# Kernel optimization log

Measured on AMD Instinct MI355X. Metric: run time of the kernel, lower is better.

## Reference

```python
import jax, jax.numpy as jnp
import numpy as np

DIM = 2048
HV = 32          # num value heads
HK = 16          # num key heads
DK = 128         # head_k_dim
DV = 128         # head_v_dim
KW = 4           # conv kernel width
KEY_DIM = HK * DK            # 2048
VAL_DIM = HV * DV            # 4096
CONV_DIM = 2 * KEY_DIM + VAL_DIM  # 8192
EPS = 1e-6
B, T = 2, 2048


def setup_inputs() -> dict:
    key = jax.random.key(0)
    ks = jax.random.split(key, 10)
    s = 0.02
    x = jax.random.normal(ks[0], (B, T, DIM), jnp.float32)
    W_qkv = jax.random.normal(ks[1], (DIM, CONV_DIM), jnp.float32) * s
    W_z = jax.random.normal(ks[2], (DIM, VAL_DIM), jnp.float32) * s
    W_a = jax.random.normal(ks[3], (DIM, HV), jnp.float32) * s
    W_b = jax.random.normal(ks[4], (DIM, HV), jnp.float32) * s
    W_out = jax.random.normal(ks[5], (VAL_DIM, DIM), jnp.float32) * s
    conv_w = jax.random.normal(ks[6], (CONV_DIM, KW), jnp.float32) * 0.2
    A_log = jnp.log(jax.random.uniform(ks[7], (HV,), jnp.float32, 1e-3, 16.0))
    dt_bias = jnp.ones((HV,), jnp.float32)
    norm_weight = jnp.ones((DV,), jnp.float32)
    return {"x": x, "W_qkv": W_qkv, "W_z": W_z, "W_a": W_a, "W_b": W_b,
            "W_out": W_out, "conv_w": conv_w, "dt_bias": dt_bias,
            "A_log": A_log, "norm_weight": norm_weight}


def _l2norm(t):
    return t * jax.lax.rsqrt(jnp.sum(t * t, axis=-1, keepdims=True) + EPS)


def _forward(x, W_qkv, W_z, W_a, W_b, W_out, conv_w, dt_bias, A_log, norm_weight):
    Bb, Tt, _ = x.shape
    mixed = x @ W_qkv                       # [B,T,CONV_DIM]
    z = x @ W_z                             # [B,T,VAL_DIM]
    a = x @ W_a                             # [B,T,HV]
    b = x @ W_b                             # [B,T,HV]

    # depthwise causal conv1d (left pad KW-1) + silu
    xp = jnp.pad(mixed, ((0, 0), (KW - 1, 0), (0, 0)))
    conv = sum(xp[:, i:i + Tt, :] * conv_w[:, i] for i in range(KW))
    mixed = jax.nn.silu(conv)

    q, k, v = jnp.split(mixed, [KEY_DIM, 2 * KEY_DIM], axis=-1)
    q = q.reshape(Bb, Tt, HK, DK)
    k = k.reshape(Bb, Tt, HK, DK)
    v = v.reshape(Bb, Tt, HV, DV)
    rep = HV // HK
    q = jnp.repeat(q, rep, axis=2)          # [B,T,HV,DK]
    k = jnp.repeat(k, rep, axis=2)

    # decay / beta
    beta = jax.nn.sigmoid(b)                                    # [B,T,HV]
    g = -jnp.exp(A_log) * jax.nn.softplus(a + dt_bias)          # [B,T,HV], < 0

    # qk l2norm in kernel + scale
    q = _l2norm(q) * (DK ** -0.5)
    k = _l2norm(k)

    # gated delta rule recurrence, time-major scan
    qT = q.transpose(1, 0, 2, 3)
    kT = k.transpose(1, 0, 2, 3)
    vT = v.transpose(1, 0, 2, 3)
    gT = g.transpose(1, 0, 2)
    bT = beta.transpose(1, 0, 2)
    S0 = jnp.zeros((Bb, HV, DK, DV), jnp.float32)

    def step(S, inp):
        qt, kt, vt, gt, bt = inp
        S = S * jnp.exp(gt)[..., None, None]
        pred = jnp.einsum('bhk,bhkv->bhv', kt, S)
        u = (vt - pred) * bt[..., None]
        S = S + jnp.einsum('bhk,bhv->bhkv', kt, u)
        o = jnp.einsum('bhk,bhkv->bhv', qt, S)
        return S, o

    _, oT = jax.lax.scan(step, S0, (qT, kT, vT, gT, bT))
    o = oT.transpose(1, 0, 2, 3)            # [B,T,HV,DV]

    # gated RMSNorm over head_v_dim: weight * rmsnorm(o) * silu(z)
    var = jnp.mean(o * o, axis=-1, keepdims=True)
    on = o * jax.lax.rsqrt(var + EPS) * norm_weight
    zg = z.reshape(Bb, Tt, HV, DV)
    on = on * jax.nn.silu(zg)

    return on.reshape(Bb, Tt, VAL_DIM) @ W_out


def reference(x, W_qkv, W_z, W_a, W_b, W_out, conv_w, dt_bias, A_log, norm_weight):
    return _forward(x, W_qkv, W_z, W_a, W_b, W_out, conv_w, dt_bias, A_log, norm_weight)
```

## Files before the change

kernel.cpp:

```cpp
#include <hip/hip_runtime.h>
#include <hip/hip_bf16.h>
#include <cstdint>
#include <cstddef>

#define DIM_ 2048
#define HV_ 32
#define HK_ 16
#define DK_ 128
#define DV_ 128
#define KW_ 4
#define KEY_DIM_ 2048
#define VAL_DIM_ 4096
#define CONV_DIM_ 8192
#define B_ 2
#define T_ 2048
#define BT_ 4096
#define CH_ 64
#define NC_ (T_ / CH_)

typedef short s8v __attribute__((ext_vector_type(8)));
typedef float f4v __attribute__((ext_vector_type(4)));

__device__ __forceinline__ unsigned short f2b(float f) {
    union { float f; unsigned u; } c; c.f = f;
    unsigned u = c.u;
    return (unsigned short)((u + 0x7fffu + ((u >> 16) & 1u)) >> 16);
}
__device__ __forceinline__ float b2f(unsigned short s) {
    union { unsigned u; float f; } c; c.u = ((unsigned)s) << 16;
    return c.f;
}
__device__ __forceinline__ unsigned int pk2(float a, float b) {
    return (unsigned)f2b(a) | ((unsigned)f2b(b) << 16);
}
__device__ __forceinline__ float silu(float x) { return x / (1.f + expf(-x)); }

__global__ void cast_bf16_k(const float* __restrict__ in, unsigned short* __restrict__ out, int n8) {
    int i = blockIdx.x * blockDim.x + threadIdx.x;
    if (i >= n8) return;
    int base = i * 8;
    f4v a = *(const f4v*)(in + base);
    f4v b = *(const f4v*)(in + base + 4);
    s8v o;
    o[0] = (short)f2b(a[0]); o[1] = (short)f2b(a[1]); o[2] = (short)f2b(a[2]); o[3] = (short)f2b(a[3]);
    o[4] = (short)f2b(b[0]); o[5] = (short)f2b(b[1]); o[6] = (short)f2b(b[2]); o[7] = (short)f2b(b[3]);
    *(s8v*)(out + base) = o;
}

__global__ void transpose_cast_k(const float* __restrict__ in, unsigned short* __restrict__ out,
                                 int R, int C) {
    __shared__ float tile[32][33];
    int c0 = blockIdx.x * 32, r0 = blockIdx.y * 32;
    int tx = threadIdx.x & 31, ty = threadIdx.x >> 5;
#pragma unroll
    for (int j = 0; j < 32; j += 8)
        tile[ty + j][tx] = in[(size_t)(r0 + ty + j) * C + c0 + tx];
    __syncthreads();
#pragma unroll
    for (int j = 0; j < 32; j += 8)
        out[(size_t)(c0 + ty + j) * R + r0 + tx] = f2b(tile[tx][ty + j]);
}

template <int OUT_BF16>
__global__ __launch_bounds__(256) void gemm_bt_k(const unsigned short* __restrict__ A,
                                                 const unsigned short* __restrict__ BT,
                                                 void* __restrict__ Cv,
                                                 int M, int N, int K) {
    __shared__ __attribute__((aligned(16))) unsigned short As[128 * 64];
    __shared__ __attribute__((aligned(16))) unsigned short Bs[128 * 64];
    const int tid = threadIdx.x;
    const int wid = tid >> 6, lane = tid & 63;
    const int wm = wid >> 1, wn = wid & 1;
    const int m0 = blockIdx.y * 128, n0 = blockIdx.x * 128;

    f4v acc[4][4];
#pragma unroll
    for (int i = 0; i < 4; i++)
#pragma unroll
        for (int j = 0; j < 4; j++) acc[i][j] = (f4v){0.f, 0.f, 0.f, 0.f};

    const int rowA = tid >> 3;
    const int cb   = (tid & 7) << 4;

    for (int kt = 0; kt < K; kt += 64) {
#pragma unroll
        for (int i = 0; i < 4; i++) {
            int row = i * 32 + rowA;
            int scb = cb ^ ((row & 7) << 4);
            const unsigned short* ga = A  + (size_t)(m0 + row) * K + kt + (scb >> 1);
            const unsigned short* gb = BT + (size_t)(n0 + row) * K + kt + (scb >> 1);
            char* la = (char*)As + i * 4096 + (wid << 10);
            char* lb = (char*)Bs + i * 4096 + (wid << 10);
            __builtin_amdgcn_global_load_lds(
                (const __attribute__((address_space(1))) unsigned int*)ga,
                (__attribute__((address_space(3))) unsigned int*)la, 16, 0, 0);
            __builtin_amdgcn_global_load_lds(
                (const __attribute__((address_space(1))) unsigned int*)gb,
                (__attribute__((address_space(3))) unsigned int*)lb, 16, 0, 0);
        }
        __syncthreads();
#pragma unroll
        for (int kk = 0; kk < 2; kk++) {
            s8v af[4], bfr[4];
#pragma unroll
            for (int mi = 0; mi < 4; mi++) {
                int row = wm * 64 + mi * 16 + (lane & 15);
                int byteoff = (row << 7) + ((kk * 64 + ((lane >> 4) << 4)) ^ ((row & 7) << 4));
                af[mi] = *(const s8v*)((const char*)As + byteoff);
            }
#pragma unroll
            for (int ni = 0; ni < 4; ni++) {
                int row = wn * 64 + ni * 16 + (lane & 15);
                int byteoff = (row << 7) + ((kk * 64 + ((lane >> 4) << 4)) ^ ((row & 7) << 4));
                bfr[ni] = *(const s8v*)((const char*)Bs + byteoff);
            }
#pragma unroll
            for (int mi = 0; mi < 4; mi++)
#pragma unroll
                for (int ni = 0; ni < 4; ni++)
                    acc[mi][ni] = __builtin_amdgcn_mfma_f32_16x16x32_bf16(
                        af[mi], bfr[ni], acc[mi][ni], 0, 0, 0);
        }
        __syncthreads();
    }
#pragma unroll
    for (int mi = 0; mi < 4; mi++) {
#pragma unroll
        for (int ni = 0; ni < 4; ni++) {
            int row = m0 + wm * 64 + mi * 16 + ((lane >> 4) << 2);
            int col = n0 + wn * 64 + ni * 16 + (lane & 15);
#pragma unroll
            for (int r = 0; r < 4; r++) {
                float v = acc[mi][ni][r];
                if (OUT_BF16)
                    ((unsigned short*)Cv)[(size_t)(row + r) * N + col] = f2b(v);
                else
                    ((float*)Cv)[(size_t)(row + r) * N + col] = v;
            }
        }
    }
}

__global__ __launch_bounds__(256) void ab_gbeta_k(const float* __restrict__ x,
                                                  const float* __restrict__ Wa,
                                                  const float* __restrict__ Wb,
                                                  const float* __restrict__ dt_bias,
                                                  const float* __restrict__ A_log,
                                                  float* __restrict__ g, float* __restrict__ beta) {
    __shared__ float xr0[16 * 513];
    const int tid = threadIdx.x;
    const int r = tid & 15, cc = tid >> 4;
    const int row0 = blockIdx.x * 16;
    float a0 = 0.f, a1 = 0.f, b0 = 0.f, b1 = 0.f;
    for (int kc = 0; kc < 2048; kc += 512) {
#pragma unroll
        for (int q = 0; q < 8; q++) {
            int f = q * 256 + tid;
            int rw = f >> 7, cl = (f & 127) << 2;
            *(f4v*)&xr0[rw * 513 + cl] = *(const f4v*)(x + (size_t)(row0 + rw) * 2048 + kc + cl);
        }
        __syncthreads();
#pragma unroll 8
        for (int k = 0; k < 512; k++) {
            float xv = xr0[r * 513 + k];
            size_t kk = (size_t)(kc + k) * 32;
            a0 += xv * Wa[kk + cc];
            a1 += xv * Wa[kk + cc + 16];
            b0 += xv * Wb[kk + cc];
            b1 += xv * Wb[kk + cc + 16];
        }
        __syncthreads();
    }
    int row = row0 + r;
    float av0 = a0 + dt_bias[cc], av1 = a1 + dt_bias[cc + 16];
    float sp0 = (av0 > 20.f) ? av0 : log1pf(expf(av0));
    float sp1 = (av1 > 20.f) ? av1 : log1pf(expf(av1));
    g[(size_t)row * 32 + cc]      = -expf(A_log[cc]) * sp0;
    g[(size_t)row * 32 + cc + 16] = -expf(A_log[cc + 16]) * sp1;
    beta[(size_t)row * 32 + cc]      = 1.f / (1.f + expf(-b0));
    beta[(size_t)row * 32 + cc + 16] = 1.f / (1.f + expf(-b1));
}

__global__ __launch_bounds__(256) void conv_fused_k(const unsigned short* __restrict__ mixp,
                                                    const float* __restrict__ convw,
                                                    unsigned short* __restrict__ qn,
                                                    unsigned short* __restrict__ kn,
                                                    unsigned short* __restrict__ vv) {
    int btid = blockIdx.x;
    int t = btid & (T_ - 1);
    int c = (blockIdx.y << 9) + (threadIdx.x << 1);
    const unsigned short* base = mixp + (size_t)btid * CONV_DIM_ + c;
    unsigned m3 = *(const unsigned*)(base);
    unsigned m2 = (t >= 1) ? *(const unsigned*)(base - CONV_DIM_) : 0u;
    unsigned m1 = (t >= 2) ? *(const unsigned*)(base - 2 * CONV_DIM_) : 0u;
    unsigned m0 = (t >= 3) ? *(const unsigned*)(base - 3 * CONV_DIM_) : 0u;
    f4v w0 = *(const f4v*)(convw + (size_t)c * 4);
    f4v w1 = *(const f4v*)(convw + (size_t)c * 4 + 4);
    float v0 = b2f((unsigned short)(m3 & 0xffff)) * w0[3] + b2f((unsigned short)(m2 & 0xffff)) * w0[2]
             + b2f((unsigned short)(m1 & 0xffff)) * w0[1] + b2f((unsigned short)(m0 & 0xffff)) * w0[0];
    float v1 = b2f((unsigned short)(m3 >> 16)) * w1[3] + b2f((unsigned short)(m2 >> 16)) * w1[2]
             + b2f((unsigned short)(m1 >> 16)) * w1[1] + b2f((unsigned short)(m0 >> 16)) * w1[0];
    v0 = silu(v0); v1 = silu(v1);
    if (c < 2 * KEY_DIM_) {
        float ss = v0 * v0 + v1 * v1;
#pragma unroll
        for (int m = 1; m < 64; m <<= 1) ss += __shfl_xor(ss, m);
        float scale = rsqrtf(ss + 1e-6f);
        int head = (c >> 7) & 15, d = c & 127;
        if (c < KEY_DIM_) {
            scale *= 0.08838834764831845f;
            *(unsigned*)(qn + ((size_t)btid * HK_ + head) * DK_ + d) = pk2(v0 * scale, v1 * scale);
        } else {
            *(unsigned*)(kn + ((size_t)btid * HK_ + head) * DK_ + d) = pk2(v0 * scale, v1 * scale);
        }
    } else {
        *(unsigned*)(vv + (size_t)btid * VAL_DIM_ + (c - 2 * KEY_DIM_)) = pk2(v0, v1);
    }
}

__global__ __launch_bounds__(256) void chunk_pre_k(
    const unsigned short* __restrict__ qn, const unsigned short* __restrict__ kn,
    unsigned short* __restrict__ vv,
    const float* __restrict__ g, const float* __restrict__ beta,
    unsigned short* __restrict__ Wg, unsigned short* __restrict__ Aog,
    unsigned short* __restrict__ knT, float* __restrict__ expG, float* __restrict__ expGr)
{
    const int c = blockIdx.x, h = blockIdx.y, b = blockIdx.z;
    const int hk = h >> 1;
    const int tid = threadIdx.x, wid = tid >> 6, lane = tid & 63;
    const int r15 = lane & 15, g4 = lane >> 4;

    __shared__ __attribute__((aligned(16))) unsigned short Klds[64 * 128];
    __shared__ __attribute__((aligned(16))) unsigned short Xlds[128 * 64];
    __shared__ float AT[64][68];
    __shared__ float STmp[16][17];
    __shared__ float Gl[64], Bl[64], EG[64];

    const size_t t0 = (size_t)b * T_ + (size_t)c * 64;
    const size_t cbk = ((size_t)(b * 32 + h) * 32 + c);

#pragma unroll
    for (int p = 0; p < 4; p++) {
        int row = p * 16 + (tid >> 4);
        int colB = (tid & 15) << 4;
        int sw = colB ^ ((row & 7) << 4);
        s8v kv = *(const s8v*)(kn + ((t0 + row) * HK_ + hk) * DK_ + (colB >> 1));
        *(s8v*)((char*)Klds + row * 256 + sw) = kv;
        s8v qv = *(const s8v*)(qn + ((t0 + row) * HK_ + hk) * DK_ + (colB >> 1));
        *(s8v*)((char*)Xlds + row * 256 + sw) = qv;
    }
    if (tid < 64) {
        Gl[tid] = g[(t0 + tid) * HV_ + h];
        Bl[tid] = beta[(t0 + tid) * HV_ + h];
    }
    __syncthreads();
    if (tid == 0) {
        float s = 0.f;
        for (int i = 0; i < 64; i++) { s += Gl[i]; Gl[i] = s; }
    }
    __syncthreads();
    if (tid < 64) {
        float Gi = Gl[tid], Gn = Gl[63];
        float e1 = expf(Gi), e2 = expf(Gn - Gi);
        EG[tid] = e1;
        expG[cbk * 64 + tid] = e1;
        expGr[cbk * 64 + tid] = e2;
    }
    __syncthreads();

    f4v kkv[4], qkv[4];
#pragma unroll
    for (int jt = 0; jt < 4; jt++) { kkv[jt] = (f4v){0,0,0,0}; qkv[jt] = (f4v){0,0,0,0}; }
    const int arow = wid * 16 + r15;
#pragma unroll
    for (int ks = 0; ks < 4; ks++) {
        int abyte = arow * 256 + ((ks * 64 + (g4 << 4)) ^ ((arow & 7) << 4));
        s8v ak = *(const s8v*)((const char*)Klds + abyte);
        s8v aq = *(const s8v*)((const char*)Xlds + abyte);
#pragma unroll
        for (int jt = 0; jt < 4; jt++) {
            int jrow = jt * 16 + r15;
            int bbyte = jrow * 256 + ((ks * 64 + (g4 << 4)) ^ ((jrow & 7) << 4));
            s8v bk = *(const s8v*)((const char*)Klds + bbyte);
            kkv[jt] = __builtin_amdgcn_mfma_f32_16x16x32_bf16(ak, bk, kkv[jt], 0, 0, 0);
            qkv[jt] = __builtin_amdgcn_mfma_f32_16x16x32_bf16(aq, bk, qkv[jt], 0, 0, 0);
        }
    }
#pragma unroll
    for (int jt = 0; jt < 4; jt++) {
#pragma unroll
        for (int r = 0; r < 4; r++) {
            int i = wid * 16 + g4 * 4 + r;
            int j = jt * 16 + r15;
            float em = expf(fminf(Gl[i] - Gl[j], 0.f));
            AT[i][j] = (j < i) ? Bl[i] * em * kkv[jt][r] : 0.f;
            float ao = (j <= i) ? em * qkv[jt][r] : 0.f;
            Aog[cbk * 4096 + i * 64 + j] = f2b(ao);
        }
    }
    __syncthreads();

    for (int u = tid; u < 1024; u += 256) {
        int row = u >> 4, v0i = (u & 15) << 3;
        s8v vx = *(const s8v*)(vv + (t0 + row) * VAL_DIM_ + h * 128 + v0i);
        float bt = Bl[row];
#pragma unroll
        for (int e = 0; e < 8; e++) {
            int v = v0i + e;
            *(unsigned short*)((char*)Xlds + v * 128 + ((row * 2) ^ ((v & 7) << 4))) =
                f2b(b2f((unsigned short)vx[e]) * bt);
        }
    }
    if ((h & 1) == 0) {
        int dk = tid & 127, th = (tid >> 7) << 5;
        size_t basek = ((size_t)(b * 16 + hk) * 128 + dk) * (size_t)T_ + (size_t)c * 64 + th;
#pragma unroll
        for (int t8 = 0; t8 < 4; t8++) {
            s8v kv;
#pragma unroll
            for (int e = 0; e < 8; e++) {
                int tt = th + t8 * 8 + e;
                kv[e] = (short)*(const unsigned short*)((const char*)Klds + tt * 256 + ((dk * 2) ^ ((tt & 7) << 4)));
            }
            *(s8v*)(knT + basek + t8 * 8) = kv;
        }
    }
    __syncthreads();

    if (lane < 16) {
        int r0 = wid * 16, col = lane;
#pragma unroll
        for (int i = 0; i < 16; i++) {
            float s = 0.f;
            for (int j = 0; j < i; j++) s += AT[r0 + i][r0 + j] * AT[r0 + j][r0 + col];
            AT[r0 + i][r0 + col] = ((col == i) ? 1.f : 0.f) - s;
        }
    }
    __syncthreads();

    {
        int ii = tid >> 4, jj = tid & 15;
        for (int I = 1; I < 4; I++)
            for (int J = 0; J < I; J++) {
                float s = 0.f;
                for (int K = J; K < I; K++) {
#pragma unroll
                    for (int m = 0; m < 16; m++)
                        s += AT[16 * I + ii][16 * K + m] * AT[16 * K + m][16 * J + jj];
                }
                STmp[ii][jj] = s;
                __syncthreads();
                float y = 0.f;
#pragma unroll
                for (int m = 0; m < 16; m++) y += AT[16 * I + ii][16 * I + m] * STmp[m][jj];
                __syncthreads();
                AT[16 * I + ii][16 * J + jj] = -y;
                __syncthreads();
            }
    }

    f4v tb[8];
#pragma unroll
    for (int vt = 0; vt < 8; vt++) tb[vt] = (f4v){0,0,0,0};
#pragma unroll
    for (int ks = 0; ks < 2; ks++) {
        s8v ta;
#pragma unroll
        for (int e = 0; e < 8; e++) ta[e] = (short)f2b(AT[arow][ks * 32 + g4 * 8 + e]);
#pragma unroll
        for (int vt = 0; vt < 8; vt++) {
            int v = vt * 16 + r15;
            int bbyte = v * 128 + ((ks * 64 + (g4 << 4)) ^ ((v & 7) << 4));
            s8v bv = *(const s8v*)((const char*)Xlds + bbyte);
            tb[vt] = __builtin_amdgcn_mfma_f32_16x16x32_bf16(ta, bv, tb[vt], 0, 0, 0);
        }
    }
#pragma unroll
    for (int vt = 0; vt < 8; vt++)
#pragma unroll
        for (int r = 0; r < 4; r++) {
            int i = wid * 16 + g4 * 4 + r, v = vt * 16 + r15;
            vv[(t0 + i) * VAL_DIM_ + h * 128 + v] = f2b(tb[vt][r]);
        }
    __syncthreads();

    {
        int dk = tid & 127;
        int tb0 = (tid >> 7) << 5;
#pragma unroll
        for (int t8 = 0; t8 < 4; t8++) {
            int tbase = tb0 + t8 * 8;
            s8v kw;
#pragma unroll
            for (int e = 0; e < 8; e++) {
                int t = tbase + e;
                float kv = b2f(*(const unsigned short*)((const char*)Klds + t * 256 + ((dk * 2) ^ ((t & 7) << 4))));
                kw[e] = (short)f2b(kv * Bl[t] * EG[t]);
            }
            *(s8v*)((char*)Xlds + dk * 128 + ((tbase * 2) ^ ((dk & 7) << 4))) = kw;
        }
    }
    __syncthreads();

    f4v wm[8];
#pragma unroll
    for (int dt = 0; dt < 8; dt++) wm[dt] = (f4v){0,0,0,0};
#pragma unroll
    for (int ks = 0; ks < 2; ks++) {
        s8v ta;
#pragma unroll
        for (int e = 0; e < 8; e++) ta[e] = (short)f2b(AT[arow][ks * 32 + g4 * 8 + e]);
#pragma unroll
        for (int dt = 0; dt < 8; dt++) {
            int dkr = dt * 16 + r15;
            int bbyte = dkr * 128 + ((ks * 64 + (g4 << 4)) ^ ((dkr & 7) << 4));
            s8v bw = *(const s8v*)((const char*)Xlds + bbyte);
            wm[dt] = __builtin_amdgcn_mfma_f32_16x16x32_bf16(ta, bw, wm[dt], 0, 0, 0);
        }
    }
#pragma unroll
    for (int dt = 0; dt < 8; dt++)
#pragma unroll
        for (int r = 0; r < 4; r++) {
            int i = wid * 16 + g4 * 4 + r, dk = dt * 16 + r15;
            Wg[cbk * 8192 + i * 128 + dk] = f2b(wm[dt][r]);
        }
}

__global__ __launch_bounds__(256) void chunk_scan_k(
    const unsigned short* __restrict__ qn, const unsigned short* __restrict__ knT,
    const unsigned short* __restrict__ tbv,
    const unsigned short* __restrict__ Wg, const unsigned short* __restrict__ Aog,
    const float* __restrict__ expG, const float* __restrict__ expGr,
    unsigned short* __restrict__ ob)
{
    const int bx = blockIdx.x;
    const int vq = bx & 3, h = (bx >> 2) & 31, b = bx >> 7;
    const int hk = h >> 1;
    const int tid = threadIdx.x, wid = tid >> 6, lane = tid & 63;
    const int r15 = lane & 15, g4 = lane >> 4;

    __shared__ __attribute__((aligned(16))) unsigned short Slds[32 * 128];
    __shared__ __attribute__((aligned(16))) unsigned short Ulds[32 * 64];
    __shared__ __attribute__((aligned(16))) unsigned short Uplds[32 * 64];

    f4v S[2][2];
#pragma unroll
    for (int i = 0; i < 2; i++)
#pragma unroll
        for (int j = 0; j < 2; j++) S[i][j] = (f4v){0,0,0,0};

    for (int c = 0; c < NC_; c++) {
        const size_t cbk = ((size_t)(b * 32 + h) * 32 + c);
        const size_t t0 = (size_t)b * T_ + (size_t)c * 64;

#pragma unroll
        for (int dkt = 0; dkt < 2; dkt++)
#pragma unroll
            for (int vt = 0; vt < 2; vt++) {
                int v = vt * 16 + r15;
                int dkb = ((wid * 2 + dkt) * 16 + g4 * 4) * 2;
                int sw = (v & 7) << 4;
                *(unsigned int*)((char*)Slds + v * 256 + ((dkb) ^ sw))     = pk2(S[dkt][vt][0], S[dkt][vt][1]);
                *(unsigned int*)((char*)Slds + v * 256 + ((dkb + 4) ^ sw)) = pk2(S[dkt][vt][2], S[dkt][vt][3]);
            }
        __syncthreads();

        f4v P[2]; P[0] = (f4v){0,0,0,0}; P[1] = (f4v){0,0,0,0};
        s8v sf[4][2];
        const unsigned short* wp = Wg + cbk * 8192 + (size_t)(wid * 16 + r15) * 128;
#pragma unroll
        for (int ks = 0; ks < 4; ks++) {
            s8v aw = *(const s8v*)(wp + ks * 32 + g4 * 8);
#pragma unroll
            for (int vt = 0; vt < 2; vt++) {
                int v = vt * 16 + r15;
                sf[ks][vt] = *(const s8v*)((const char*)Slds + v * 256 + ((ks * 64 + g4 * 16) ^ ((v & 7) << 4)));
                P[vt] = __builtin_amdgcn_mfma_f32_16x16x32_bf16(aw, sf[ks][vt], P[vt], 0, 0, 0);
            }
        }
        float egr[4];
#pragma unroll
        for (int r = 0; r < 4; r++) egr[r] = expGr[cbk * 64 + wid * 16 + g4 * 4 + r];
#pragma unroll
        for (int vt = 0; vt < 2; vt++) {
            float uu[4], up[4];
#pragma unroll
            for (int r = 0; r < 4; r++) {
                int t = wid * 16 + g4 * 4 + r;
                unsigned short tv = tbv[(t0 + t) * VAL_DIM_ + h * 128 + vq * 32 + vt * 16 + r15];
                uu[r] = b2f(tv) - P[vt][r];
                up[r] = uu[r] * egr[r];
            }
            int v = vt * 16 + r15;
            int tb2 = (wid * 16 + g4 * 4) * 2;
            int sw = (v & 7) << 4;
            *(unsigned int*)((char*)Ulds  + v * 128 + ((tb2) ^ sw))     = pk2(uu[0], uu[1]);
            *(unsigned int*)((char*)Ulds  + v * 128 + ((tb2 + 4) ^ sw)) = pk2(uu[2], uu[3]);
            *(unsigned int*)((char*)Uplds + v * 128 + ((tb2) ^ sw))     = pk2(up[0], up[1]);
            *(unsigned int*)((char*)Uplds + v * 128 + ((tb2 + 4) ^ sw)) = pk2(up[2], up[3]);
        }
        __syncthreads();

        f4v O[2]; O[0] = (f4v){0,0,0,0}; O[1] = (f4v){0,0,0,0};
        float egi = expG[cbk * 64 + wid * 16 + r15];
        const unsigned short* qp = qn + ((t0 + wid * 16 + r15) * HK_ + hk) * DK_;
#pragma unroll
        for (int ks = 0; ks < 4; ks++) {
            s8v q0 = *(const s8v*)(qp + ks * 32 + g4 * 8);
            s8v qg;
#pragma unroll
            for (int e = 0; e < 8; e++) qg[e] = (short)f2b(b2f((unsigned short)q0[e]) * egi);
#pragma unroll
            for (int vt = 0; vt < 2; vt++)
                O[vt] = __builtin_amdgcn_mfma_f32_16x16x32_bf16(qg, sf[ks][vt], O[vt], 0, 0, 0);
        }
        const unsigned short* ap = Aog + cbk * 4096 + (size_t)(wid * 16 + r15) * 64;
#pragma unroll
        for (int ks = 0; ks < 2; ks++) {
            s8v aa = *(const s8v*)(ap + ks * 32 + g4 * 8);
#pragma unroll
            for (int vt = 0; vt < 2; vt++) {
                int v = vt * 16 + r15;
                s8v bu = *(const s8v*)((const char*)Ulds + v * 128 + ((ks * 64 + g4 * 16) ^ ((v & 7) << 4)));
                O[vt] = __builtin_amdgcn_mfma_f32_16x16x32_bf16(aa, bu, O[vt], 0, 0, 0);
            }
        }
#pragma unroll
        for (int vt = 0; vt < 2; vt++)
#pragma unroll
            for (int r = 0; r < 4; r++) {
                int t = c * 64 + wid * 16 + g4 * 4 + r;
                ob[((size_t)b * T_ + t) * VAL_DIM_ + h * 128 + vq * 32 + vt * 16 + r15] = f2b(O[vt][r]);
            }

        float gam = expG[cbk * 64 + 63];
#pragma unroll
        for (int dkt = 0; dkt < 2; dkt++)
#pragma unroll
            for (int vt = 0; vt < 2; vt++) {
                S[dkt][vt][0] *= gam; S[dkt][vt][1] *= gam;
                S[dkt][vt][2] *= gam; S[dkt][vt][3] *= gam;
            }
        const unsigned short* kp = knT + ((size_t)(b * 16 + hk) * 128) * (size_t)T_;
#pragma unroll
        for (int ks = 0; ks < 2; ks++) {
            s8v bu[2];
#pragma unroll
            for (int vt = 0; vt < 2; vt++) {
                int v = vt * 16 + r15;
                bu[vt] = *(const s8v*)((const char*)Uplds + v * 128 + ((ks * 64 + g4 * 16) ^ ((v & 7) << 4)));
            }
#pragma unroll
            for (int dkt = 0; dkt < 2; dkt++) {
                s8v ak = *(const s8v*)(kp + (size_t)((wid * 2 + dkt) * 16 + r15) * T_ + (size_t)c * 64 + ks * 32 + g4 * 8);
#pragma unroll
                for (int vt = 0; vt < 2; vt++)
                    S[dkt][vt] = __builtin_amdgcn_mfma_f32_16x16x32_bf16(ak, bu[vt], S[dkt][vt], 0, 0, 0);
            }
        }
        __syncthreads();
    }
}

__global__ __launch_bounds__(256) void norm_gate_k(unsigned short* __restrict__ o,
                                                   const unsigned short* __restrict__ z,
                                                   const float* __restrict__ nw) {
    int lane = threadIdx.x & 63;
    size_t bh = (size_t)blockIdx.x * 4 + (threadIdx.x >> 6);
    unsigned ov = *(unsigned*)(o + bh * 128 + lane * 2);
    float v0 = b2f((unsigned short)(ov & 0xffff)), v1 = b2f((unsigned short)(ov >> 16));
    float ss = v0 * v0 + v1 * v1;
#pragma unroll
    for (int m = 1; m < 64; m <<= 1) ss += __shfl_xor(ss, m);
    float rr = rsqrtf(ss * (1.f / 128.f) + 1e-6f);
    unsigned zv = *(const unsigned*)(z + bh * 128 + lane * 2);
    float z0 = b2f((unsigned short)(zv & 0xffff)), z1 = b2f((unsigned short)(zv >> 16));
    float o0 = v0 * rr * nw[lane * 2]     * silu(z0);
    float o1 = v1 * rr * nw[lane * 2 + 1] * silu(z1);
    *(unsigned*)(o + bh * 128 + lane * 2) = pk2(o0, o1);
}

extern "C" void kernel_launch(void* const* d_in, const int* in_sizes, int n_in,
                              void* d_out, int out_size, void* d_ws, size_t ws_size,
                              hipStream_t stream) {
    const float* x      = (const float*)d_in[0];
    const float* W_qkv  = (const float*)d_in[1];
    const float* W_z    = (const float*)d_in[2];
    const float* W_a    = (const float*)d_in[3];
    const float* W_b    = (const float*)d_in[4];
    const float* W_out  = (const float*)d_in[5];
    const float* conv_w = (const float*)d_in[6];
    const float* dt_bias= (const float*)d_in[7];
    const float* A_log  = (const float*)d_in[8];
    const float* norm_w = (const float*)d_in[9];

    char* w = (char*)d_ws;
    const size_t MBc = (size_t)1 << 20;
    unsigned short* mixp  = (unsigned short*)(w);
    unsigned short* Wmat  = (unsigned short*)(w);
    unsigned short* knT   = (unsigned short*)(w + 32 * MBc);
    unsigned short* Aog   = (unsigned short*)(w + 48 * MBc);
    unsigned short* WqkvT = (unsigned short*)(w + 64 * MBc);
    unsigned short* obuf  = (unsigned short*)(w + 64 * MBc);
    unsigned short* kn    = (unsigned short*)(w + 80 * MBc);
    unsigned short* WzT   = (unsigned short*)(w + 96 * MBc);
    unsigned short* WoutT = (unsigned short*)(w + 96 * MBc);
    unsigned short* xb    = (unsigned short*)(w + 112 * MBc);
    unsigned short* qn    = (unsigned short*)(w + 112 * MBc);
    unsigned short* vv    = (unsigned short*)(w + 128 * MBc);
    unsigned short* zb    = (unsigned short*)(w + 160 * MBc);
    float* gbuf  = (float*)(w + 192 * MBc);
    float* bbuf  = (float*)(w + 192 * MBc + 512 * 1024);
    float* expG  = (float*)(w + 192 * MBc + 1024 * 1024);
    float* expGr = (float*)(w + 192 * MBc + 1536 * 1024);

    cast_bf16_k<<<(BT_ * DIM_ / 8 + 255) / 256, 256, 0, stream>>>(x, xb, BT_ * DIM_ / 8);
    transpose_cast_k<<<dim3(CONV_DIM_ / 32, DIM_ / 32), 256, 0, stream>>>(W_qkv, WqkvT, DIM_, CONV_DIM_);
    transpose_cast_k<<<dim3(VAL_DIM_ / 32, DIM_ / 32), 256, 0, stream>>>(W_z, WzT, DIM_, VAL_DIM_);
    gemm_bt_k<1><<<dim3(CONV_DIM_ / 128, BT_ / 128), 256, 0, stream>>>(xb, WqkvT, mixp, BT_, CONV_DIM_, DIM_);
    gemm_bt_k<1><<<dim3(VAL_DIM_ / 128, BT_ / 128), 256, 0, stream>>>(xb, WzT, zb, BT_, VAL_DIM_, DIM_);
    transpose_cast_k<<<dim3(DIM_ / 32, VAL_DIM_ / 32), 256, 0, stream>>>(W_out, WoutT, VAL_DIM_, DIM_);
    ab_gbeta_k<<<BT_ / 16, 256, 0, stream>>>(x, W_a, W_b, dt_bias, A_log, gbuf, bbuf);
    conv_fused_k<<<dim3(BT_, CONV_DIM_ / 512), 256, 0, stream>>>(mixp, conv_w, qn, kn, vv);
    chunk_pre_k<<<dim3(NC_, HV_, B_), 256, 0, stream>>>(qn, kn, vv, gbuf, bbuf,
                                                        Wmat, Aog, knT, expG, expGr);
    chunk_scan_k<<<B_ * HV_ * 4, 256, 0, stream>>>(qn, knT, vv, Wmat, Aog, expG, expGr, obuf);
    norm_gate_k<<<BT_ * HV_ / 4, 256, 0, stream>>>(obuf, zb, norm_w);
    gemm_bt_k<0><<<dim3(DIM_ / 128, BT_ / 128), 256, 0, stream>>>(obuf, WoutT, d_out, BT_, DIM_, VAL_DIM_);
}
```

Baseline: 754.2 us.

## Prefetch next chunk operands in scan, fuse x cast into ab_gbeta, split QKV GEMM

The chunk scan loop is restructured to load the next chunk's global operands (W, A, k, q, v, decay factors) into registers while the current chunk computes, using two alternating operand sets. One __syncthreads per chunk is removed by moving a barrier. The bf16 cast of x is folded into ab_gbeta_k so the separate cast kernel disappears, and the QKV GEMM is launched as two half-width launches. Double-buffered registers raise VGPR pressure and may reduce occupancy, and the barrier removal needs the LDS reuse ordering to stay correct.

```diff
diff --git a/kernel.cpp b/kernel.cpp
--- a/kernel.cpp
+++ b/kernel.cpp
@@ -35,18 +35,6 @@
 }
 __device__ __forceinline__ float silu(float x) { return x / (1.f + expf(-x)); }
 
-__global__ void cast_bf16_k(const float* __restrict__ in, unsigned short* __restrict__ out, int n8) {
-    int i = blockIdx.x * blockDim.x + threadIdx.x;
-    if (i >= n8) return;
-    int base = i * 8;
-    f4v a = *(const f4v*)(in + base);
-    f4v b = *(const f4v*)(in + base + 4);
-    s8v o;
-    o[0] = (short)f2b(a[0]); o[1] = (short)f2b(a[1]); o[2] = (short)f2b(a[2]); o[3] = (short)f2b(a[3]);
-    o[4] = (short)f2b(b[0]); o[5] = (short)f2b(b[1]); o[6] = (short)f2b(b[2]); o[7] = (short)f2b(b[3]);
-    *(s8v*)(out + base) = o;
-}
-
 __global__ void transpose_cast_k(const float* __restrict__ in, unsigned short* __restrict__ out,
                                  int R, int C) {
     __shared__ float tile[32][33];
@@ -146,7 +134,8 @@
                                                   const float* __restrict__ Wb,
                                                   const float* __restrict__ dt_bias,
                                                   const float* __restrict__ A_log,
-                                                  float* __restrict__ g, float* __restrict__ beta) {
+                                                  float* __restrict__ g, float* __restrict__ beta,
+                                                  unsigned short* __restrict__ xb) {
     __shared__ float xr0[16 * 513];
     const int tid = threadIdx.x;
     const int r = tid & 15, cc = tid >> 4;
@@ -157,7 +146,11 @@
         for (int q = 0; q < 8; q++) {
             int f = q * 256 + tid;
             int rw = f >> 7, cl = (f & 127) << 2;
-            *(f4v*)&xr0[rw * 513 + cl] = *(const f4v*)(x + (size_t)(row0 + rw) * 2048 + kc + cl);
+            f4v xv = *(const f4v*)(x + (size_t)(row0 + rw) * 2048 + kc + cl);
+            *(f4v*)&xr0[rw * 513 + cl] = xv;
+            unsigned long long p = (unsigned long long)pk2(xv[0], xv[1])
+                                 | ((unsigned long long)pk2(xv[2], xv[3]) << 32);
+            *(unsigned long long*)(xb + (size_t)(row0 + rw) * 2048 + kc + cl) = p;
         }
         __syncthreads();
 #pragma unroll 8
@@ -450,10 +443,46 @@
 #pragma unroll
         for (int j = 0; j < 2; j++) S[i][j] = (f4v){0,0,0,0};
 
-    for (int c = 0; c < NC_; c++) {
+    struct ScanOps {
+        s8v aw[4], aa[2], ak[4], q0[4];
+        float tv[8], egr4[4], egi, gam;
+    };
+    ScanOps opA, opB;
+
+    const unsigned short* kpbase = knT + ((size_t)(b * 16 + hk) * 128) * (size_t)T_;
+
+    auto scan_load = [&](ScanOps& o, int c) {
         const size_t cbk = ((size_t)(b * 32 + h) * 32 + c);
         const size_t t0 = (size_t)b * T_ + (size_t)c * 64;
-
+        const unsigned short* wp = Wg + cbk * 8192 + (size_t)(wid * 16 + r15) * 128;
+#pragma unroll
+        for (int ks = 0; ks < 4; ks++) o.aw[ks] = *(const s8v*)(wp + ks * 32 + g4 * 8);
+        const unsigned short* ap = Aog + cbk * 4096 + (size_t)(wid * 16 + r15) * 64;
+#pragma unroll
+        for (int ks = 0; ks < 2; ks++) o.aa[ks] = *(const s8v*)(ap + ks * 32 + g4 * 8);
+#pragma unroll
+        for (int ks = 0; ks < 2; ks++)
+#pragma unroll
+            for (int dkt = 0; dkt < 2; dkt++)
+                o.ak[ks * 2 + dkt] = *(const s8v*)(kpbase +
+                    (size_t)((wid * 2 + dkt) * 16 + r15) * T_ + (size_t)c * 64 + ks * 32 + g4 * 8);
+        const unsigned short* qp = qn + ((t0 + wid * 16 + r15) * HK_ + hk) * DK_;
+#pragma unroll
+        for (int ks = 0; ks < 4; ks++) o.q0[ks] = *(const s8v*)(qp + ks * 32 + g4 * 8);
+#pragma unroll
+        for (int vt = 0; vt < 2; vt++)
+#pragma unroll
+            for (int r = 0; r < 4; r++) {
+                int t = wid * 16 + g4 * 4 + r;
+                o.tv[vt * 4 + r] = b2f(tbv[(t0 + t) * VAL_DIM_ + h * 128 + vq * 32 + vt * 16 + r15]);
+            }
+#pragma unroll
+        for (int r = 0; r < 4; r++) o.egr4[r] = expGr[cbk * 64 + wid * 16 + g4 * 4 + r];
+        o.egi = expG[cbk * 64 + wid * 16 + r15];
+        o.gam = expG[cbk * 64 + 63];
+    };
+
+    auto body = [&](ScanOps& o, int c) {
 #pragma unroll
         for (int dkt = 0; dkt < 2; dkt++)
 #pragma unroll
@@ -468,29 +497,21 @@
 
         f4v P[2]; P[0] = (f4v){0,0,0,0}; P[1] = (f4v){0,0,0,0};
         s8v sf[4][2];
-        const unsigned short* wp = Wg + cbk * 8192 + (size_t)(wid * 16 + r15) * 128;
-#pragma unroll
-        for (int ks = 0; ks < 4; ks++) {
-            s8v aw = *(const s8v*)(wp + ks * 32 + g4 * 8);
+#pragma unroll
+        for (int ks = 0; ks < 4; ks++)
 #pragma unroll
             for (int vt = 0; vt < 2; vt++) {
                 int v = vt * 16 + r15;
                 sf[ks][vt] = *(const s8v*)((const char*)Slds + v * 256 + ((ks * 64 + g4 * 16) ^ ((v & 7) << 4)));
-                P[vt] = __builtin_amdgcn_mfma_f32_16x16x32_bf16(aw, sf[ks][vt], P[vt], 0, 0, 0);
-            }
-        }
-        float egr[4];
-#pragma unroll
-        for (int r = 0; r < 4; r++) egr[r] = expGr[cbk * 64 + wid * 16 + g4 * 4 + r];
+                P[vt] = __builtin_amdgcn_mfma_f32_16x16x32_bf16(o.aw[ks], sf[ks][vt], P[vt], 0, 0, 0);
+            }
 #pragma unroll
         for (int vt = 0; vt < 2; vt++) {
             float uu[4], up[4];
 #pragma unroll
             for (int r = 0; r < 4; r++) {
-                int t = wid * 16 + g4 * 4 + r;
-                unsigned short tv = tbv[(t0 + t) * VAL_DIM_ + h * 128 + vq * 32 + vt * 16 + r15];
-                uu[r] = b2f(tv) - P[vt][r];
-                up[r] = uu[r] * egr[r];
+                uu[r] = o.tv[vt * 4 + r] - P[vt][r];
+                up[r] = uu[r] * o.egr4[r];
             }
             int v = vt * 16 + r15;
             int tb2 = (wid * 16 + g4 * 4) * 2;
@@ -500,32 +521,27 @@
             *(unsigned int*)((char*)Uplds + v * 128 + ((tb2) ^ sw))     = pk2(up[0], up[1]);
             *(unsigned int*)((char*)Uplds + v * 128 + ((tb2 + 4) ^ sw)) = pk2(up[2], up[3]);
         }
-        __syncthreads();
 
         f4v O[2]; O[0] = (f4v){0,0,0,0}; O[1] = (f4v){0,0,0,0};
-        float egi = expG[cbk * 64 + wid * 16 + r15];
-        const unsigned short* qp = qn + ((t0 + wid * 16 + r15) * HK_ + hk) * DK_;
 #pragma unroll
         for (int ks = 0; ks < 4; ks++) {
-            s8v q0 = *(const s8v*)(qp + ks * 32 + g4 * 8);
             s8v qg;
 #pragma unroll
-            for (int e = 0; e < 8; e++) qg[e] = (short)f2b(b2f((unsigned short)q0[e]) * egi);
+            for (int e = 0; e < 8; e++) qg[e] = (short)f2b(b2f((unsigned short)o.q0[ks][e]) * o.egi);
 #pragma unroll
             for (int vt = 0; vt < 2; vt++)
                 O[vt] = __builtin_amdgcn_mfma_f32_16x16x32_bf16(qg, sf[ks][vt], O[vt], 0, 0, 0);
         }
-        const unsigned short* ap = Aog + cbk * 4096 + (size_t)(wid * 16 + r15) * 64;
-#pragma unroll
-        for (int ks = 0; ks < 2; ks++) {
-            s8v aa = *(const s8v*)(ap + ks * 32 + g4 * 8);
+        __syncthreads();
+
+#pragma unroll
+        for (int ks = 0; ks < 2; ks++)
 #pragma unroll
             for (int vt = 0; vt < 2; vt++) {
                 int v = vt * 16 + r15;
                 s8v bu = *(const s8v*)((const char*)Ulds + v * 128 + ((ks * 64 + g4 * 16) ^ ((v & 7) << 4)));
-                O[vt] = __builtin_amdgcn_mfma_f32_16x16x32_bf16(aa, bu, O[vt], 0, 0, 0);
-            }
-        }
+                O[vt] = __builtin_amdgcn_mfma_f32_16x16x32_bf16(o.aa[ks], bu, O[vt], 0, 0, 0);
+            }
 #pragma unroll
         for (int vt = 0; vt < 2; vt++)
 #pragma unroll
@@ -534,15 +550,13 @@
                 ob[((size_t)b * T_ + t) * VAL_DIM_ + h * 128 + vq * 32 + vt * 16 + r15] = f2b(O[vt][r]);
             }
 
-        float gam = expG[cbk * 64 + 63];
 #pragma unroll
         for (int dkt = 0; dkt < 2; dkt++)
 #pragma unroll
             for (int vt = 0; vt < 2; vt++) {
-                S[dkt][vt][0] *= gam; S[dkt][vt][1] *= gam;
-                S[dkt][vt][2] *= gam; S[dkt][vt][3] *= gam;
-            }
-        const unsigned short* kp = knT + ((size_t)(b * 16 + hk) * 128) * (size_t)T_;
+                S[dkt][vt][0] *= o.gam; S[dkt][vt][1] *= o.gam;
+                S[dkt][vt][2] *= o.gam; S[dkt][vt][3] *= o.gam;
+            }
 #pragma unroll
         for (int ks = 0; ks < 2; ks++) {
             s8v bu[2];
@@ -552,14 +566,19 @@
                 bu[vt] = *(const s8v*)((const char*)Uplds + v * 128 + ((ks * 64 + g4 * 16) ^ ((v & 7) << 4)));
             }
 #pragma unroll
-            for (int dkt = 0; dkt < 2; dkt++) {
-                s8v ak = *(const s8v*)(kp + (size_t)((wid * 2 + dkt) * 16 + r15) * T_ + (size_t)c * 64 + ks * 32 + g4 * 8);
+            for (int dkt = 0; dkt < 2; dkt++)
 #pragma unroll
                 for (int vt = 0; vt < 2; vt++)
-                    S[dkt][vt] = __builtin_amdgcn_mfma_f32_16x16x32_bf16(ak, bu[vt], S[dkt][vt], 0, 0, 0);
-            }
-        }
-        __syncthreads();
+                    S[dkt][vt] = __builtin_amdgcn_mfma_f32_16x16x32_bf16(o.ak[ks * 2 + dkt], bu[vt], S[dkt][vt], 0, 0, 0);
+        }
+    };
+
+    scan_load(opA, 0);
+    for (int c = 0; c < NC_; c += 2) {
+        scan_load(opB, (c + 1 < NC_) ? c + 1 : c);
+        body(opA, c);
+        if (c + 2 < NC_) scan_load(opA, c + 2);
+        body(opB, c + 1);
     }
 }
 
@@ -615,13 +634,14 @@
     float* expG  = (float*)(w + 192 * MBc + 1024 * 1024);
     float* expGr = (float*)(w + 192 * MBc + 1536 * 1024);
 
-    cast_bf16_k<<<(BT_ * DIM_ / 8 + 255) / 256, 256, 0, stream>>>(x, xb, BT_ * DIM_ / 8);
+    ab_gbeta_k<<<BT_ / 16, 256, 0, stream>>>(x, W_a, W_b, dt_bias, A_log, gbuf, bbuf, xb);
     transpose_cast_k<<<dim3(CONV_DIM_ / 32, DIM_ / 32), 256, 0, stream>>>(W_qkv, WqkvT, DIM_, CONV_DIM_);
     transpose_cast_k<<<dim3(VAL_DIM_ / 32, DIM_ / 32), 256, 0, stream>>>(W_z, WzT, DIM_, VAL_DIM_);
-    gemm_bt_k<1><<<dim3(CONV_DIM_ / 128, BT_ / 128), 256, 0, stream>>>(xb, WqkvT, mixp, BT_, CONV_DIM_, DIM_);
+    gemm_bt_k<1><<<dim3(CONV_DIM_ / 256, BT_ / 128), 256, 0, stream>>>(xb, WqkvT, mixp, BT_, CONV_DIM_, DIM_);
+    gemm_bt_k<1><<<dim3(CONV_DIM_ / 256, BT_ / 128), 256, 0, stream>>>(
+        xb, WqkvT + (size_t)(CONV_DIM_ / 2) * DIM_, mixp + CONV_DIM_ / 2, BT_, CONV_DIM_, DIM_);
     gemm_bt_k<1><<<dim3(VAL_DIM_ / 128, BT_ / 128), 256, 0, stream>>>(xb, WzT, zb, BT_, VAL_DIM_, DIM_);
     transpose_cast_k<<<dim3(DIM_ / 32, VAL_DIM_ / 32), 256, 0, stream>>>(W_out, WoutT, VAL_DIM_, DIM_);
-    ab_gbeta_k<<<BT_ / 16, 256, 0, stream>>>(x, W_a, W_b, dt_bias, A_log, gbuf, bbuf);
     conv_fused_k<<<dim3(BT_, CONV_DIM_ / 512), 256, 0, stream>>>(mixp, conv_w, qn, kn, vv);
     chunk_pre_k<<<dim3(NC_, HV_, B_), 256, 0, stream>>>(qn, kn, vv, gbuf, bbuf,
                                                         Wmat, Aog, knT, expG, expGr);
```

New measurement: 763.9 us. Within noise of the previous version (+1.3%).
